# Optimization experiments

Hardware: AMD Instinct MI355X
Metric: run time of the kernel (lower is better)

## Reference

```python
import jax, jax.numpy as jnp
import numpy as np

N = 100_000      # nodes
E = 1_600_000    # edges
F_IN = 128       # node_features
H1, H2 = 50, 20  # GCLSTM hidden sizes (fixed in the model)


def _norm_weights(src, dst, w, n):
    # PyG get_laplacian(sym): remove self loops, deg over row, sym-normalize.
    w = jnp.where(src == dst, jnp.zeros_like(w), w)  # remove self-loops (weight 0)
    deg = jax.ops.segment_sum(w, src, num_segments=n)
    deg_safe = jnp.where(deg > 0, deg, jnp.ones_like(deg))
    dis = jnp.where(deg > 0, deg_safe ** -0.5, jnp.zeros_like(deg))
    return dis[src] * w * dis[dst]


def _lhat_matvec(x, src, dst, wn, n):
    # L_hat = 2*L/lambda_max - I with sym norm and lambda_max=2  =>  -D^-1/2 A D^-1/2
    return -jax.ops.segment_sum(wn[:, None] * x[src], dst, num_segments=n)


def _gclstm_cell(x, src, dst, wn, n, Wx, bx, theta, bconv, out_ch):
    # One GCLSTM step with H = C = 0 (the model passes H=C=None).
    H = jnp.zeros((n, out_ch), x.dtype)
    C = jnp.zeros((n, out_ch), x.dtype)
    # ChebConv(H) for all 4 gates: Tx_0 = H, Tx_1 = L_hat @ H   (K = 2)
    Tx = jnp.stack([H, _lhat_matvec(H, src, dst, wn, n)])       # [2, n, out]
    conv = jnp.einsum('knf,gkfo->gno', Tx, theta) + bconv[:, None, :]  # [4, n, out]
    Z = x @ Wx + bx                                              # [n, 4*out], gates i,f,c,o
    zi, zf, zc, zo = jnp.split(Z, 4, axis=-1)
    I = jax.nn.sigmoid(zi + conv[0])
    Fg = jax.nn.sigmoid(zf + conv[1])
    T = jnp.tanh(zc + conv[2])
    C = Fg * C + I * T
    O = jax.nn.sigmoid(zo + conv[3])
    return O * jnp.tanh(C)


def setup_inputs() -> dict:
    key = jax.random.key(0)
    ks = jax.random.split(key, 14)
    s = 0.1  # param init scale
    return {
        'x': jax.random.normal(ks[0], (N, F_IN), jnp.float32),
        'edge_index': jax.random.randint(ks[1], (2, E), 0, N, dtype=jnp.int32),
        'edge_weight': jax.random.uniform(ks[2], (E,), jnp.float32),
        # layer 1: W_x for gates i,f,c,o concatenated, Cheb thetas [gate, K, in, out]
        'Wx1': s * jax.random.normal(ks[3], (F_IN, 4 * H1), jnp.float32),
        'bx1': s * jax.random.normal(ks[4], (4 * H1,), jnp.float32),
        'theta1': s * jax.random.normal(ks[5], (4, 2, H1, H1), jnp.float32),
        'bconv1': s * jax.random.normal(ks[6], (4, H1), jnp.float32),
        # layer 2
        'Wx2': s * jax.random.normal(ks[7], (H1, 4 * H2), jnp.float32),
        'bx2': s * jax.random.normal(ks[8], (4 * H2,), jnp.float32),
        'theta2': s * jax.random.normal(ks[9], (4, 2, H2, H2), jnp.float32),
        'bconv2': s * jax.random.normal(ks[10], (4, H2), jnp.float32),
        # linear head
        'Wl': s * jax.random.normal(ks[11], (H2, 1), jnp.float32),
        'bl': s * jax.random.normal(ks[12], (1,), jnp.float32),
    }


def reference(x, edge_index, edge_weight, Wx1, bx1, theta1, bconv1,
              Wx2, bx2, theta2, bconv2, Wl, bl):
    src, dst = edge_index[0], edge_index[1]
    wn = _norm_weights(src, dst, edge_weight, N)
    h = _gclstm_cell(x, src, dst, wn, N, Wx1, bx1, theta1, bconv1, H1)
    h = _gclstm_cell(h, src, dst, wn, N, Wx2, bx2, theta2, bconv2, H2)
    h = jax.nn.relu(h)
    # F.dropout: identity at inference (deterministic baseline)
    return h @ Wl + bl  # [N, 1]
```

## Files before the change

### kernel.cpp

```cpp
#include <hip/hip_runtime.h>
#include <hip/hip_bf16.h>


#define NODES 100000
#define NTILES 6250

typedef float v4f   __attribute__((ext_vector_type(4)));
typedef float fragC __attribute__((ext_vector_type(4)));
typedef short frag8 __attribute__((ext_vector_type(8)));

#define OFF_B1H 0
#define OFF_B2H 40960
#define OFF_PB1 49152
#define OFF_PB2 49792

__device__ __forceinline__ unsigned short f2bf(float f) {
  unsigned int u = __float_as_uint(f);
  u += 0x7fffu + ((u >> 16) & 1u);
  return (unsigned short)(u >> 16);
}
__device__ __forceinline__ float fsig(float z) {
  float t = __builtin_amdgcn_exp2f(z * -1.44269504088896f);
  return __builtin_amdgcn_rcpf(1.0f + t);
}
__device__ __forceinline__ float ftanh(float z) {
  float t = __builtin_amdgcn_exp2f(z * 2.88539008177793f);
  return 1.0f - 2.0f * __builtin_amdgcn_rcpf(t + 1.0f);
}

union bfu { __hip_bfloat162 h; unsigned int u; };

__device__ __forceinline__ frag8 cvt8hi(const float* v) {
  frag8 hi;
#pragma unroll
  for (int p = 0; p < 4; ++p) {
    bfu c; c.h = __float22bfloat162_rn(make_float2(v[2 * p], v[2 * p + 1]));
    hi[2 * p]     = (short)(c.u & 0xffffu);
    hi[2 * p + 1] = (short)(c.u >> 16);
  }
  return hi;
}
__device__ __forceinline__ void cvt8(const float* v, frag8& hi, frag8& lo) {
  float lof[8];
#pragma unroll
  for (int p = 0; p < 4; ++p) {
    bfu c; c.h = __float22bfloat162_rn(make_float2(v[2 * p], v[2 * p + 1]));
    hi[2 * p]     = (short)(c.u & 0xffffu);
    hi[2 * p + 1] = (short)(c.u >> 16);
    lof[2 * p]     = v[2 * p]     - __uint_as_float((c.u & 0xffffu) << 16);
    lof[2 * p + 1] = v[2 * p + 1] - __uint_as_float(c.u & 0xffff0000u);
  }
#pragma unroll
  for (int p = 0; p < 4; ++p) {
    bfu c; c.h = __float22bfloat162_rn(make_float2(lof[2 * p], lof[2 * p + 1]));
    lo[2 * p]     = (short)(c.u & 0xffffu);
    lo[2 * p + 1] = (short)(c.u >> 16);
  }
}

__global__ void pack_weights(const float* __restrict__ Wx1, const float* __restrict__ bx1,
                             const float* __restrict__ bconv1,
                             const float* __restrict__ Wx2, const float* __restrict__ bx2,
                             const float* __restrict__ bconv2,
                             unsigned char* __restrict__ ws) {
  const int tid = blockIdx.x * blockDim.x + threadIdx.x;
  const int stride = gridDim.x * blockDim.x;
  unsigned short* B1H = (unsigned short*)(ws + OFF_B1H);
  unsigned short* B2H = (unsigned short*)(ws + OFF_B2H);
  float* PB1 = (float*)(ws + OFF_PB1);
  float* PB2 = (float*)(ws + OFF_PB2);

  for (int idx = tid; idx < 20480; idx += stride) {
    int j = idx & 7, lane = (idx >> 3) & 63, ft = idx >> 9;
    int s = ft / 10, t = ft % 10;
    int k = 32 * s + ((lane >> 4) << 3) + j;
    int m = lane & 15;
    int c = -1, g = 0;
    if (t <= 8) { g = t % 3; c = 16 * (t / 3) + m; }
    else if (m < 6) { c = 48 + m / 3; g = m % 3; }
    float val = 0.f;
    if (c >= 0) {
      int gs = (g == 0) ? 0 : (g == 1) ? 2 : 3;
      val = Wx1[k * 200 + gs * 50 + c];
    }
    B1H[idx] = f2bf(val);
  }
  for (int idx = tid; idx < 4096; idx += stride) {
    int j = idx & 7, lane = (idx >> 3) & 63, ft = idx >> 9;
    int s = ft >> 2, t = ft & 3;
    int k = 32 * s + ((lane >> 4) << 3) + j;
    int m = lane & 15;
    int c = -1, g = 0;
    if (t <= 2) { g = t; c = m; }
    else if (m < 12) { c = 16 + m / 3; g = m % 3; }
    float val = 0.f;
    if (c >= 0 && k < 50) {
      int gs = (g == 0) ? 0 : (g == 1) ? 2 : 3;
      val = Wx2[k * 80 + gs * 20 + c];
    }
    B2H[idx] = f2bf(val);
  }
  for (int idx = tid; idx < 160; idx += stride) {
    int t = idx >> 4, m = idx & 15;
    int c = -1, g = 0;
    if (t <= 8) { g = t % 3; c = 16 * (t / 3) + m; }
    else if (m < 6) { c = 48 + m / 3; g = m % 3; }
    float v = 0.f;
    if (c >= 0) {
      int gs = (g == 0) ? 0 : (g == 1) ? 2 : 3;
      v = bx1[gs * 50 + c] + bconv1[gs * 50 + c];
    }
    PB1[idx] = v;
  }
  for (int idx = tid; idx < 64; idx += stride) {
    int t = idx >> 4, m = idx & 15;
    int c = -1, g = 0;
    if (t <= 2) { g = t; c = m; }
    else if (m < 12) { c = 16 + m / 3; g = m % 3; }
    float v = 0.f;
    if (c >= 0) {
      int gs = (g == 0) ? 0 : (g == 1) ? 2 : 3;
      v = bx2[gs * 20 + c] + bconv2[gs * 20 + c];
    }
    PB2[idx] = v;
  }
}

__global__ __launch_bounds__(256, 2) void gclstm_main(
    const float* __restrict__ x, const unsigned char* __restrict__ wsb,
    const float* __restrict__ Wl, const float* __restrict__ bl,
    float* __restrict__ out) {
  __shared__ unsigned short sH[4][16 * 72];
  __shared__ float sP[4][16 * 36];
  __shared__ float sT[4][16 * 12];

  const int tid = threadIdx.x;
  const int lane = tid & 63;
  const int wave = tid >> 6;
  const int m = lane & 15;
  const int q = lane >> 4;
  const int tau = blockIdx.x * 4 + wave;
  if (tau >= NTILES) return;

  unsigned short* sHw = (unsigned short*)sH + wave * (16 * 72);
  float* sPw = (float*)sP + wave * (16 * 36);
  float* sTw = (float*)sT + wave * (16 * 12);

  {
    int r0 = lane >> 2, c0 = 48 + (lane & 3) * 4;
    *(unsigned long long*)(sHw + r0 * 72 + c0) = 0ull;
  }
#pragma unroll
  for (int i = 0; i < 3; ++i) {
    int idx = lane * 3 + i;
    sPw[(idx / 12) * 36 + 20 + idx % 12] = 0.f;
  }

  const float* xr = x + (size_t)(tau * 16 + m) * 128 + q * 8;
  v4f xb[8];
#pragma unroll
  for (int s = 0; s < 4; ++s) {
    xb[2 * s] = *(const v4f*)(xr + 32 * s);
    xb[2 * s + 1] = *(const v4f*)(xr + 32 * s + 4);
  }

  const float* pb1 = (const float*)(wsb + OFF_PB1);
  const float* pb2 = (const float*)(wsb + OFF_PB2);
  float bias1v[10], bias2v[4];
#pragma unroll
  for (int t = 0; t < 10; ++t) bias1v[t] = pb1[16 * t + m];
#pragma unroll
  for (int t = 0; t < 4; ++t) bias2v[t] = pb2[16 * t + m];

  const frag8* g1 = (const frag8*)(wsb + OFF_B1H);
  const frag8* g2 = (const frag8*)(wsb + OFF_B2H);

  frag8 ba[10], bb[10];
#pragma unroll
  for (int t = 0; t < 10; ++t) ba[t] = g1[t * 64 + lane];

  frag8 ah[4];
#pragma unroll
  for (int s = 0; s < 4; ++s) {
    float av[8];
    *(v4f*)av = xb[2 * s];
    *(v4f*)(av + 4) = xb[2 * s + 1];
    ah[s] = cvt8hi(av);
  }

  fragC acc[10];
#pragma unroll
  for (int t = 0; t < 10; ++t)
    acc[t] = (fragC){bias1v[t], bias1v[t], bias1v[t], bias1v[t]};
#pragma unroll
  for (int s = 0; s < 4; ++s) {
    frag8* bc = (s & 1) ? bb : ba;
    frag8* bn = (s & 1) ? ba : bb;
    if (s < 3) {
#pragma unroll
      for (int t = 0; t < 10; ++t) bn[t] = g1[((s + 1) * 10 + t) * 64 + lane];
    }
#pragma unroll
    for (int t = 0; t < 10; ++t)
      acc[t] = __builtin_amdgcn_mfma_f32_16x16x32_bf16(ah[s], bc[t], acc[t], 0, 0, 0);
    __builtin_amdgcn_sched_barrier(0);
  }

  frag8 b2f[8];
#pragma unroll
  for (int i = 0; i < 8; ++i) b2f[i] = g2[i * 64 + lane];

#pragma unroll
  for (int b = 0; b < 3; ++b)
#pragma unroll
    for (int r = 0; r < 4; ++r) {
      float I = fsig(acc[3 * b][r]);
      float T = ftanh(acc[3 * b + 1][r]);
      float O = fsig(acc[3 * b + 2][r]);
      sHw[(q * 4 + r) * 72 + 16 * b + m] = f2bf(O * ftanh(I * T));
    }
  if (m < 6) {
#pragma unroll
    for (int r = 0; r < 4; ++r) sTw[(q * 4 + r) * 6 + m] = acc[9][r];
  }
  {
    int row = lane & 15, cc = lane >> 4;
    if (cc < 2) {
      float I = fsig(sTw[row * 6 + 3 * cc]);
      float T = ftanh(sTw[row * 6 + 3 * cc + 1]);
      float O = fsig(sTw[row * 6 + 3 * cc + 2]);
      sHw[row * 72 + 48 + cc] = f2bf(O * ftanh(I * T));
    }
  }

  frag8 hh[2];
#pragma unroll
  for (int s = 0; s < 2; ++s)
    hh[s] = *(const frag8*)(sHw + m * 72 + 32 * s + 8 * q);
  fragC acc2[4];
#pragma unroll
  for (int t = 0; t < 4; ++t)
    acc2[t] = (fragC){bias2v[t], bias2v[t], bias2v[t], bias2v[t]};
#pragma unroll
  for (int s = 0; s < 2; ++s)
#pragma unroll
    for (int t = 0; t < 4; ++t)
      acc2[t] = __builtin_amdgcn_mfma_f32_16x16x32_bf16(hh[s], b2f[s * 4 + t], acc2[t], 0, 0, 0);

  const float wlm = Wl[m];
  const float wlc = Wl[16 + q];
#pragma unroll
  for (int r = 0; r < 4; ++r) {
    float I = fsig(acc2[0][r]);
    float T = ftanh(acc2[1][r]);
    float O = fsig(acc2[2][r]);
    float h2 = O * ftanh(I * T);
    sPw[(q * 4 + r) * 36 + m] = fmaxf(h2, 0.f) * wlm;
  }
  if (m < 12) {
#pragma unroll
    for (int r = 0; r < 4; ++r) sTw[(q * 4 + r) * 12 + m] = acc2[3][r];
  }
  {
    int row = lane & 15, cc = lane >> 4;
    float I = fsig(sTw[row * 12 + 3 * cc]);
    float T = ftanh(sTw[row * 12 + 3 * cc + 1]);
    float O = fsig(sTw[row * 12 + 3 * cc + 2]);
    float h2 = O * ftanh(I * T);
    sPw[row * 36 + 16 + cc] = fmaxf(h2, 0.f) * wlc;
  }

  float pv[8];
  *(v4f*)pv       = *(const v4f*)(sPw + m * 36 + q * 8);
  *(v4f*)(pv + 4) = *(const v4f*)(sPw + m * 36 + q * 8 + 4);
  frag8 pa, pl;
  cvt8(pv, pa, pl);
  frag8 bw;
#pragma unroll
  for (int j = 0; j < 8; ++j)
    bw[j] = (short)((m == 0 && (8 * q + j) < 20) ? 0x3F80 : 0);
  fragC acco = (fragC){0.f, 0.f, 0.f, 0.f};
  acco = __builtin_amdgcn_mfma_f32_16x16x32_bf16(pa, bw, acco, 0, 0, 0);
  acco = __builtin_amdgcn_mfma_f32_16x16x32_bf16(pl, bw, acco, 0, 0, 0);

  if (m == 0) {
    const float blv = bl[0];
    v4f res;
#pragma unroll
    for (int r = 0; r < 4; ++r) res[r] = acco[r] + blv;
    *(v4f*)(out + tau * 16 + 4 * q) = res;
  }
}

extern "C" void kernel_launch(void* const* d_in, const int* in_sizes, int n_in,
                              void* d_out, int out_size, void* d_ws, size_t ws_size,
                              hipStream_t stream) {
  (void)in_sizes; (void)n_in; (void)out_size; (void)ws_size;
  const float* x = (const float*)d_in[0];
  const float* Wx1 = (const float*)d_in[3];
  const float* bx1 = (const float*)d_in[4];
  const float* bconv1 = (const float*)d_in[6];
  const float* Wx2 = (const float*)d_in[7];
  const float* bx2 = (const float*)d_in[8];
  const float* bconv2 = (const float*)d_in[10];
  const float* Wl = (const float*)d_in[11];
  const float* bl = (const float*)d_in[12];
  unsigned char* ws = (unsigned char*)d_ws;

  hipLaunchKernelGGL(pack_weights, dim3(32), dim3(256), 0, stream,
                     Wx1, bx1, bconv1, Wx2, bx2, bconv2, ws);
  hipLaunchKernelGGL(gclstm_main, dim3((NTILES + 3) / 4), dim3(256), 0, stream,
                     x, ws, Wl, bl, (float*)d_out);
}
```

Baseline: 128.8 us.

## Process two 16-row tiles per wave to reuse layer-1 weight fragments

Each wave now handles two consecutive 16-node tiles instead of one, so the grid is halved. The layer-1 and layer-2 weight fragments loaded from the workspace are shared across both tiles, which halves per-node weight load traffic and interleaves twice as many independent MFMAs. In exchange, register pressure roughly doubles (two x buffers, two sets of 10 accumulators) and LDS use grows, which may cut occupancy under launch_bounds(256,2) or cause spills.

New measurement: 129.4 us. No clear change (+0.5%).

```diff
diff --git a/kernel.cpp b/kernel.cpp
--- a/kernel.cpp
+++ b/kernel.cpp
@@ -4,6 +4,7 @@
 
 #define NODES 100000
 #define NTILES 6250
+#define NJOBS 3125
 
 typedef float v4f   __attribute__((ext_vector_type(4)));
 typedef float fragC __attribute__((ext_vector_type(4)));
@@ -130,25 +131,27 @@
     const float* __restrict__ x, const unsigned char* __restrict__ wsb,
     const float* __restrict__ Wl, const float* __restrict__ bl,
     float* __restrict__ out) {
-  __shared__ unsigned short sH[4][16 * 72];
+  __shared__ unsigned short sH[4][2][16 * 72];
   __shared__ float sP[4][16 * 36];
-  __shared__ float sT[4][16 * 12];
+  __shared__ float sT[4][2][16 * 12];
 
   const int tid = threadIdx.x;
   const int lane = tid & 63;
   const int wave = tid >> 6;
   const int m = lane & 15;
   const int q = lane >> 4;
-  const int tau = blockIdx.x * 4 + wave;
-  if (tau >= NTILES) return;
-
-  unsigned short* sHw = (unsigned short*)sH + wave * (16 * 72);
+  const int job = blockIdx.x * 4 + wave;
+  if (job >= NJOBS) return;
+  const int tau0 = job * 2;
+
+  unsigned short* sHw = (unsigned short*)sH + wave * (2 * 16 * 72);
   float* sPw = (float*)sP + wave * (16 * 36);
-  float* sTw = (float*)sT + wave * (16 * 12);
+  float* sTw = (float*)sT + wave * (2 * 16 * 12);
 
   {
     int r0 = lane >> 2, c0 = 48 + (lane & 3) * 4;
     *(unsigned long long*)(sHw + r0 * 72 + c0) = 0ull;
+    *(unsigned long long*)(sHw + 16 * 72 + r0 * 72 + c0) = 0ull;
   }
 #pragma unroll
   for (int i = 0; i < 3; ++i) {
@@ -156,13 +159,26 @@
     sPw[(idx / 12) * 36 + 20 + idx % 12] = 0.f;
   }
 
-  const float* xr = x + (size_t)(tau * 16 + m) * 128 + q * 8;
-  v4f xb[8];
-#pragma unroll
-  for (int s = 0; s < 4; ++s) {
-    xb[2 * s] = *(const v4f*)(xr + 32 * s);
-    xb[2 * s + 1] = *(const v4f*)(xr + 32 * s + 4);
-  }
+  const float* xr0 = x + (size_t)(tau0 * 16 + m) * 128 + q * 8;
+  const float* xr1 = xr0 + 16 * 128;
+  v4f xb0[8], xb1[8];
+#pragma unroll
+  for (int s = 0; s < 4; ++s) {
+    xb0[2 * s] = *(const v4f*)(xr0 + 32 * s);
+    xb0[2 * s + 1] = *(const v4f*)(xr0 + 32 * s + 4);
+  }
+#pragma unroll
+  for (int s = 0; s < 4; ++s) {
+    xb1[2 * s] = *(const v4f*)(xr1 + 32 * s);
+    xb1[2 * s + 1] = *(const v4f*)(xr1 + 32 * s + 4);
+  }
+
+  const frag8* g1 = (const frag8*)(wsb + OFF_B1H);
+  const frag8* g2 = (const frag8*)(wsb + OFF_B2H);
+
+  frag8 ba[10], bb[10];
+#pragma unroll
+  for (int t = 0; t < 10; ++t) ba[t] = g1[t * 64 + lane];
 
   const float* pb1 = (const float*)(wsb + OFF_PB1);
   const float* pb2 = (const float*)(wsb + OFF_PB2);
@@ -172,26 +188,28 @@
 #pragma unroll
   for (int t = 0; t < 4; ++t) bias2v[t] = pb2[16 * t + m];
 
-  const frag8* g1 = (const frag8*)(wsb + OFF_B1H);
-  const frag8* g2 = (const frag8*)(wsb + OFF_B2H);
-
-  frag8 ba[10], bb[10];
-#pragma unroll
-  for (int t = 0; t < 10; ++t) ba[t] = g1[t * 64 + lane];
-
-  frag8 ah[4];
+  frag8 ah0[4], ah1[4];
 #pragma unroll
   for (int s = 0; s < 4; ++s) {
     float av[8];
-    *(v4f*)av = xb[2 * s];
-    *(v4f*)(av + 4) = xb[2 * s + 1];
-    ah[s] = cvt8hi(av);
-  }
-
-  fragC acc[10];
-#pragma unroll
-  for (int t = 0; t < 10; ++t)
-    acc[t] = (fragC){bias1v[t], bias1v[t], bias1v[t], bias1v[t]};
+    *(v4f*)av = xb0[2 * s];
+    *(v4f*)(av + 4) = xb0[2 * s + 1];
+    ah0[s] = cvt8hi(av);
+  }
+#pragma unroll
+  for (int s = 0; s < 4; ++s) {
+    float av[8];
+    *(v4f*)av = xb1[2 * s];
+    *(v4f*)(av + 4) = xb1[2 * s + 1];
+    ah1[s] = cvt8hi(av);
+  }
+
+  fragC acc0[10], acc1[10];
+#pragma unroll
+  for (int t = 0; t < 10; ++t) {
+    acc0[t] = (fragC){bias1v[t], bias1v[t], bias1v[t], bias1v[t]};
+    acc1[t] = acc0[t];
+  }
 #pragma unroll
   for (int s = 0; s < 4; ++s) {
     frag8* bc = (s & 1) ? bb : ba;
@@ -202,7 +220,10 @@
     }
 #pragma unroll
     for (int t = 0; t < 10; ++t)
-      acc[t] = __builtin_amdgcn_mfma_f32_16x16x32_bf16(ah[s], bc[t], acc[t], 0, 0, 0);
+      acc0[t] = __builtin_amdgcn_mfma_f32_16x16x32_bf16(ah0[s], bc[t], acc0[t], 0, 0, 0);
+#pragma unroll
+    for (int t = 0; t < 10; ++t)
+      acc1[t] = __builtin_amdgcn_mfma_f32_16x16x32_bf16(ah1[s], bc[t], acc1[t], 0, 0, 0);
     __builtin_amdgcn_sched_barrier(0);
   }
 
@@ -211,84 +232,95 @@
   for (int i = 0; i < 8; ++i) b2f[i] = g2[i * 64 + lane];
 
 #pragma unroll
-  for (int b = 0; b < 3; ++b)
-#pragma unroll
-    for (int r = 0; r < 4; ++r) {
-      float I = fsig(acc[3 * b][r]);
-      float T = ftanh(acc[3 * b + 1][r]);
-      float O = fsig(acc[3 * b + 2][r]);
-      sHw[(q * 4 + r) * 72 + 16 * b + m] = f2bf(O * ftanh(I * T));
-    }
-  if (m < 6) {
-#pragma unroll
-    for (int r = 0; r < 4; ++r) sTw[(q * 4 + r) * 6 + m] = acc[9][r];
-  }
-  {
-    int row = lane & 15, cc = lane >> 4;
-    if (cc < 2) {
-      float I = fsig(sTw[row * 6 + 3 * cc]);
-      float T = ftanh(sTw[row * 6 + 3 * cc + 1]);
-      float O = fsig(sTw[row * 6 + 3 * cc + 2]);
-      sHw[row * 72 + 48 + cc] = f2bf(O * ftanh(I * T));
-    }
-  }
-
-  frag8 hh[2];
-#pragma unroll
-  for (int s = 0; s < 2; ++s)
-    hh[s] = *(const frag8*)(sHw + m * 72 + 32 * s + 8 * q);
-  fragC acc2[4];
-#pragma unroll
-  for (int t = 0; t < 4; ++t)
-    acc2[t] = (fragC){bias2v[t], bias2v[t], bias2v[t], bias2v[t]};
-#pragma unroll
-  for (int s = 0; s < 2; ++s)
-#pragma unroll
-    for (int t = 0; t < 4; ++t)
-      acc2[t] = __builtin_amdgcn_mfma_f32_16x16x32_bf16(hh[s], b2f[s * 4 + t], acc2[t], 0, 0, 0);
+  for (int tt = 0; tt < 2; ++tt) {
+    const fragC* ac = tt ? acc1 : acc0;
+    unsigned short* sHt = sHw + tt * (16 * 72);
+    float* sTt = sTw + tt * (16 * 12);
+#pragma unroll
+    for (int b = 0; b < 3; ++b)
+#pragma unroll
+      for (int r = 0; r < 4; ++r) {
+        float I = fsig(ac[3 * b][r]);
+        float T = ftanh(ac[3 * b + 1][r]);
+        float O = fsig(ac[3 * b + 2][r]);
+        sHt[(q * 4 + r) * 72 + 16 * b + m] = f2bf(O * ftanh(I * T));
+      }
+    if (m < 6) {
+#pragma unroll
+      for (int r = 0; r < 4; ++r) sTt[(q * 4 + r) * 6 + m] = ac[9][r];
+    }
+    {
+      int row = lane & 15, cc = lane >> 4;
+      if (cc < 2) {
+        float I = fsig(sTt[row * 6 + 3 * cc]);
+        float T = ftanh(sTt[row * 6 + 3 * cc + 1]);
+        float O = fsig(sTt[row * 6 + 3 * cc + 2]);
+        sHt[row * 72 + 48 + cc] = f2bf(O * ftanh(I * T));
+      }
+    }
+  }
 
   const float wlm = Wl[m];
   const float wlc = Wl[16 + q];
-#pragma unroll
-  for (int r = 0; r < 4; ++r) {
-    float I = fsig(acc2[0][r]);
-    float T = ftanh(acc2[1][r]);
-    float O = fsig(acc2[2][r]);
-    float h2 = O * ftanh(I * T);
-    sPw[(q * 4 + r) * 36 + m] = fmaxf(h2, 0.f) * wlm;
-  }
-  if (m < 12) {
-#pragma unroll
-    for (int r = 0; r < 4; ++r) sTw[(q * 4 + r) * 12 + m] = acc2[3][r];
-  }
-  {
-    int row = lane & 15, cc = lane >> 4;
-    float I = fsig(sTw[row * 12 + 3 * cc]);
-    float T = ftanh(sTw[row * 12 + 3 * cc + 1]);
-    float O = fsig(sTw[row * 12 + 3 * cc + 2]);
-    float h2 = O * ftanh(I * T);
-    sPw[row * 36 + 16 + cc] = fmaxf(h2, 0.f) * wlc;
-  }
-
-  float pv[8];
-  *(v4f*)pv       = *(const v4f*)(sPw + m * 36 + q * 8);
-  *(v4f*)(pv + 4) = *(const v4f*)(sPw + m * 36 + q * 8 + 4);
-  frag8 pa, pl;
-  cvt8(pv, pa, pl);
-  frag8 bw;
-#pragma unroll
-  for (int j = 0; j < 8; ++j)
-    bw[j] = (short)((m == 0 && (8 * q + j) < 20) ? 0x3F80 : 0);
-  fragC acco = (fragC){0.f, 0.f, 0.f, 0.f};
-  acco = __builtin_amdgcn_mfma_f32_16x16x32_bf16(pa, bw, acco, 0, 0, 0);
-  acco = __builtin_amdgcn_mfma_f32_16x16x32_bf16(pl, bw, acco, 0, 0, 0);
-
-  if (m == 0) {
-    const float blv = bl[0];
-    v4f res;
-#pragma unroll
-    for (int r = 0; r < 4; ++r) res[r] = acco[r] + blv;
-    *(v4f*)(out + tau * 16 + 4 * q) = res;
+  const float blv = bl[0];
+#pragma unroll
+  for (int tt = 0; tt < 2; ++tt) {
+    unsigned short* sHt = sHw + tt * (16 * 72);
+    float* sTt = sTw + tt * (16 * 12);
+    frag8 hh[2];
+#pragma unroll
+    for (int s = 0; s < 2; ++s)
+      hh[s] = *(const frag8*)(sHt + m * 72 + 32 * s + 8 * q);
+    fragC acc2[4];
+#pragma unroll
+    for (int t = 0; t < 4; ++t)
+      acc2[t] = (fragC){bias2v[t], bias2v[t], bias2v[t], bias2v[t]};
+#pragma unroll
+    for (int s = 0; s < 2; ++s)
+#pragma unroll
+      for (int t = 0; t < 4; ++t)
+        acc2[t] = __builtin_amdgcn_mfma_f32_16x16x32_bf16(hh[s], b2f[s * 4 + t], acc2[t], 0, 0, 0);
+
+#pragma unroll
+    for (int r = 0; r < 4; ++r) {
+      float I = fsig(acc2[0][r]);
+      float T = ftanh(acc2[1][r]);
+      float O = fsig(acc2[2][r]);
+      float h2 = O * ftanh(I * T);
+      sPw[(q * 4 + r) * 36 + m] = fmaxf(h2, 0.f) * wlm;
+    }
+    if (m < 12) {
+#pragma unroll
+      for (int r = 0; r < 4; ++r) sTt[(q * 4 + r) * 12 + m] = acc2[3][r];
+    }
+    {
+      int row = lane & 15, cc = lane >> 4;
+      float I = fsig(sTt[row * 12 + 3 * cc]);
+      float T = ftanh(sTt[row * 12 + 3 * cc + 1]);
+      float O = fsig(sTt[row * 12 + 3 * cc + 2]);
+      float h2 = O * ftanh(I * T);
+      sPw[row * 36 + 16 + cc] = fmaxf(h2, 0.f) * wlc;
+    }
+
+    float pv[8];
+    *(v4f*)pv       = *(const v4f*)(sPw + m * 36 + q * 8);
+    *(v4f*)(pv + 4) = *(const v4f*)(sPw + m * 36 + q * 8 + 4);
+    frag8 pa, pl;
+    cvt8(pv, pa, pl);
+    frag8 bw;
+#pragma unroll
+    for (int j = 0; j < 8; ++j)
+      bw[j] = (short)((m == 0 && (8 * q + j) < 20) ? 0x3F80 : 0);
+    fragC acco = (fragC){0.f, 0.f, 0.f, 0.f};
+    acco = __builtin_amdgcn_mfma_f32_16x16x32_bf16(pa, bw, acco, 0, 0, 0);
+    acco = __builtin_amdgcn_mfma_f32_16x16x32_bf16(pl, bw, acco, 0, 0, 0);
+
+    if (m == 0) {
+      v4f res;
+#pragma unroll
+      for (int r = 0; r < 4; ++r) res[r] = acco[r] + blv;
+      *(v4f*)(out + (tau0 + tt) * 16 + 4 * q) = res;
+    }
   }
 }
 
@@ -309,6 +341,6 @@
 
   hipLaunchKernelGGL(pack_weights, dim3(32), dim3(256), 0, stream,
                      Wx1, bx1, bconv1, Wx2, bx2, bconv2, ws);
-  hipLaunchKernelGGL(gclstm_main, dim3((NTILES + 3) / 4), dim3(256), 0, stream,
+  hipLaunchKernelGGL(gclstm_main, dim3((NJOBS + 3) / 4), dim3(256), 0, stream,
                      x, ws, Wl, bl, (float*)d_out);
 }
```
